# Optimization experiments

Measured on AMD Instinct MI355X. Metric: run time of the kernel, lower is better.

The kernel has to match this reference:

```python
import math
import jax, jax.numpy as jnp
import numpy as np

B, S, D = 4, 2048, 512
N_HEADS, D_HEAD = 8, 64
NUM_BUCKETS, MAX_DIST = 32, 128


def _relative_position_bucket(relative_position, num_buckets=NUM_BUCKETS, max_distance=MAX_DIST):
    # bidirectional variant (is_decoder=False)
    num_buckets = num_buckets // 2
    rel_buckets = (relative_position > 0).astype(jnp.int32) * num_buckets
    rp = jnp.abs(relative_position)
    max_exact = num_buckets // 2
    is_small = rp < max_exact
    rp_large = max_exact + (
        jnp.log(rp.astype(jnp.float32) / max_exact)
        / math.log(max_distance / max_exact)
        * (num_buckets - max_exact)
    ).astype(jnp.int32)
    rp_large = jnp.minimum(rp_large, num_buckets - 1)
    return rel_buckets + jnp.where(is_small, rp, rp_large)


def compute_bias(rel_bias, q_len, k_len):
    ctx = jnp.arange(q_len)[:, None]
    mem = jnp.arange(k_len)[None, :]
    buckets = _relative_position_bucket(mem - ctx)           # [q, k]
    values = rel_bias[buckets]                                # [q, k, h]
    return jnp.transpose(values, (2, 0, 1))[None]             # [1, h, q, k]


def setup_inputs() -> dict:
    key = jax.random.key(0)
    ks = jax.random.split(key, 6)
    scale = 1.0 / math.sqrt(D)
    return {
        "hidden_states": jax.random.normal(ks[0], (B, S, D), jnp.float32),
        "Wq": jax.random.normal(ks[1], (D, D), jnp.float32) * scale,
        "Wk": jax.random.normal(ks[2], (D, D), jnp.float32) * scale,
        "Wv": jax.random.normal(ks[3], (D, D), jnp.float32) * scale,
        "Wo": jax.random.normal(ks[4], (D, D), jnp.float32) * scale,
        "rel_bias": jax.random.normal(ks[5], (NUM_BUCKETS, N_HEADS), jnp.float32),
    }


def reference(hidden_states, Wq, Wk, Wv, Wo, rel_bias):
    b, s, _ = hidden_states.shape
    # projections (no bias, no 1/sqrt(d) scaling — T5 style)
    q = (hidden_states @ Wq).reshape(b, s, N_HEADS, D_HEAD).transpose(0, 2, 1, 3)
    k = (hidden_states @ Wk).reshape(b, s, N_HEADS, D_HEAD).transpose(0, 2, 1, 3)
    v = (hidden_states @ Wv).reshape(b, s, N_HEADS, D_HEAD).transpose(0, 2, 1, 3)
    scores = jnp.einsum("bhqd,bhkd->bhqk", q, k)             # [b,h,s,s]
    position_bias = compute_bias(rel_bias, s, s)              # [1,h,s,s]
    scores = scores + position_bias
    attn = jax.nn.softmax(scores, axis=-1)                    # dropout: eval mode -> identity
    out = jnp.einsum("bhqk,bhkd->bhqd", attn, v)
    out = out.transpose(0, 2, 1, 3).reshape(b, s, N_HEADS * D_HEAD)
    return out @ Wo
```

## Files before the change

kernel.cpp:

```cpp
#include <hip/hip_runtime.h>
#include <stdint.h>

typedef __attribute__((ext_vector_type(8))) __bf16 bf16x8;
typedef __attribute__((ext_vector_type(4))) __bf16 bf16x4;
typedef __attribute__((ext_vector_type(8))) _Float16 f16x8;
typedef __attribute__((ext_vector_type(4))) float f32x4;
typedef __attribute__((ext_vector_type(4))) unsigned int u32x4;

#define SEQ 2048
#define LOG2E 1.4426950408889634f

#define OFF_HSF   0ull
#define OFF_AO    0ull
#define OFF_WF    8388608ull
#define OFF_WO    9961472ull
#define OFF_Q     10485760ull
#define OFF_K     18874368ull
#define OFF_VT    27262976ull
#define OFF_BIAS  35651584ull

__device__ __forceinline__ int swz(int row) { return ((row & 7) << 4) ^ ((row & 8) << 1); }

__device__ __forceinline__ void gl_lds16(const void* g, void* l) {
  __builtin_amdgcn_global_load_lds(
      (__attribute__((address_space(1))) void*)(uintptr_t)g,
      (__attribute__((address_space(3))) void*)(uint32_t)(uintptr_t)l, 16, 0, 0);
}

__device__ __forceinline__ float fast_exp2(float x) { return __builtin_amdgcn_exp2f(x); }

__global__ void k_prep(const float* __restrict__ hs,
                       const float* __restrict__ Wq, const float* __restrict__ Wk,
                       const float* __restrict__ Wv, const float* __restrict__ Wo,
                       const float* __restrict__ rel_bias,
                       _Float16* __restrict__ hsf, _Float16* __restrict__ wf,
                       __bf16* __restrict__ wo_t, float* __restrict__ bias_tab) {
  int z = blockIdx.z;
  if (z >= 4) {
    int cid = (z - 4) * 64 + blockIdx.y * 8 + blockIdx.x;
    int gid = cid * 256 + threadIdx.x;
    int row = gid >> 6, c8 = (gid & 63) * 8;
    const float* p = hs + (size_t)row * 512 + c8;
    float4 a = *(const float4*)p, b = *(const float4*)(p + 4);
    float v[8] = {a.x, a.y, a.z, a.w, b.x, b.y, b.z, b.w};
    f16x8 hv;
#pragma unroll
    for (int j = 0; j < 8; ++j) hv[j] = (_Float16)v[j];
    *(f16x8*)(hsf + (size_t)row * 512 + c8) = hv;
    return;
  }
  __shared__ float tile[64][65];
  const float* W = (z == 0) ? Wq : (z == 1) ? Wk : (z == 2) ? Wv : Wo;
  int k0 = blockIdx.y * 64, n0 = blockIdx.x * 64;
  int tx = threadIdx.x & 63, ty = threadIdx.x >> 6;
  for (int r = ty; r < 64; r += 4) tile[r][tx] = W[(size_t)(k0 + r) * 512 + n0 + tx];
  __syncthreads();
  if (z < 3) {
    float scale = (z == 0) ? LOG2E : 1.0f;
    for (int r = ty; r < 64; r += 4)
      wf[(size_t)(z * 512 + n0 + r) * 512 + k0 + tx] = (_Float16)(tile[tx][r] * scale);
  } else {
    for (int r = ty; r < 64; r += 4)
      wo_t[(size_t)(n0 + r) * 512 + k0 + tx] = (__bf16)tile[tx][r];
    int blk = blockIdx.y * 8 + blockIdx.x;
#pragma unroll
    for (int e = 0; e < 2; ++e) {
      int idx = blk * 512 + e * 256 + threadIdx.x;
      int h = idx >> 12, dIdx = idx & 4095;
      float v = 0.f;
      if (dIdx < 4095) {
        int d = dIdx - 2047;
        int rp = d < 0 ? -d : d;
        int bp;
        if (rp < 8) bp = rp;
        else bp = 8 + (rp >= 12) + (rp >= 16) + (rp >= 23) + (rp >= 32) + (rp >= 46) + (rp >= 64) + (rp >= 91);
        v = rel_bias[((d > 0 ? 16 : 0) + bp) * 8 + h] * LOG2E;
      }
      bias_tab[idx] = v;
    }
  }
}

template <int MODE, int KSTEPS, int LDA, int LDB>
__global__ __launch_bounds__(256) void k_gemm(const void* __restrict__ Ap,
                                              const void* __restrict__ Btp,
                                              _Float16* __restrict__ qf,
                                              _Float16* __restrict__ kf,
                                              __bf16* __restrict__ vt,
                                              float* __restrict__ fo) {
  __shared__ __align__(16) char As[2][128 * 32 * 2];
  __shared__ __align__(16) char Bs[2][128 * 32 * 2];
  const char* A = (const char*)Ap;
  const char* Bt = (const char*)Btp;
  int tid = threadIdx.x, w = tid >> 6, l = tid & 63;
  int lr = l & 15, lh = l >> 4;
  int nwg = gridDim.x * gridDim.y;
  int flat = blockIdx.y * gridDim.x + blockIdx.x;
  int flat2 = (flat & 7) * (nwg >> 3) + (flat >> 3);
  int m0 = (flat2 / gridDim.x) * 128, n0 = (flat2 % gridDim.x) * 128;
  int wm = (w >> 1) * 64, wn = (w & 1) * 64;
  f32x4 zero4 = {0.f, 0.f, 0.f, 0.f};
  f32x4 acc[4][4];
#pragma unroll
  for (int i = 0; i < 4; ++i)
#pragma unroll
    for (int j = 0; j < 4; ++j) acc[i][j] = zero4;

  auto stage = [&](int kt, int buf) {
#pragma unroll
    for (int c = 0; c < 2; ++c) {
      int i = c * 256 + w * 64 + l;
      int row = i >> 2, cc = i & 3;
      gl_lds16(A + ((size_t)(m0 + row) * LDA + kt * 32 + cc * 8) * 2,
               &As[buf][(c * 256 + w * 64) * 16]);
      gl_lds16(Bt + ((size_t)(n0 + row) * LDB + kt * 32 + cc * 8) * 2,
               &Bs[buf][(c * 256 + w * 64) * 16]);
    }
  };

  stage(0, 0);
  __syncthreads();
#pragma unroll 2
  for (int kt = 0; kt < KSTEPS; ++kt) {
    int cur = kt & 1;
    if (kt + 1 < KSTEPS) stage(kt + 1, cur ^ 1);
    u32x4 af[4], bfr[4];
#pragma unroll
    for (int mi = 0; mi < 4; ++mi)
      af[mi] = *(const u32x4*)&As[cur][((wm + mi * 16 + lr) * 32 + lh * 8) * 2];
#pragma unroll
    for (int ni = 0; ni < 4; ++ni)
      bfr[ni] = *(const u32x4*)&Bs[cur][((wn + ni * 16 + lr) * 32 + lh * 8) * 2];
#pragma unroll
    for (int mi = 0; mi < 4; ++mi)
#pragma unroll
      for (int ni = 0; ni < 4; ++ni) {
        if (MODE == 0)
          acc[mi][ni] = __builtin_amdgcn_mfma_f32_16x16x32_f16(
              __builtin_bit_cast(f16x8, af[mi]), __builtin_bit_cast(f16x8, bfr[ni]),
              acc[mi][ni], 0, 0, 0);
        else
          acc[mi][ni] = __builtin_amdgcn_mfma_f32_16x16x32_bf16(
              __builtin_bit_cast(bf16x8, af[mi]), __builtin_bit_cast(bf16x8, bfr[ni]),
              acc[mi][ni], 0, 0, 0);
      }
    __syncthreads();
  }

  if (MODE == 0 && n0 >= 1024) {
#pragma unroll
    for (int mi = 0; mi < 4; ++mi)
#pragma unroll
      for (int ni = 0; ni < 4; ++ni) {
        int m = m0 + wm + mi * 16 + lh * 4;
        int n = n0 + wn + ni * 16 + lr;
        int c9 = n & 511, hh = c9 >> 6, dh = c9 & 63;
        int b = m >> 11, s = m & 2047;
        int loc = s & 63;
        int pp = ((loc >> 5) << 5) | (((loc >> 2) & 3) << 3) | (((loc >> 4) & 1) << 2);
        bf16x4 o;
#pragma unroll
        for (int r = 0; r < 4; ++r) o[r] = (__bf16)acc[mi][ni][r];
        *(bf16x4*)&vt[((size_t)(b * 8 + hh) * 64 + dh) * 2048 + (s & ~63) + pp] = o;
      }
    return;
  }

#pragma unroll
  for (int mi = 0; mi < 4; ++mi)
#pragma unroll
    for (int ni = 0; ni < 4; ++ni)
#pragma unroll
      for (int r = 0; r < 4; ++r) {
        int m = m0 + wm + mi * 16 + lh * 4 + r;
        int n = n0 + wn + ni * 16 + lr;
        float vv = acc[mi][ni][r];
        if (MODE == 0) {
          int which = n >> 9, c9 = n & 511, hh = c9 >> 6, dh = c9 & 63;
          int b = m >> 11, s = m & 2047;
          size_t o = (size_t)((b * 8 + hh) * 2048 + s) * 64 + dh;
          if (which == 0) qf[o] = (_Float16)vv;
          else            kf[o] = (_Float16)vv;
        } else {
          fo[(size_t)m * 512 + n] = vv;
        }
      }
}

__global__ __launch_bounds__(512) void k_attn(const _Float16* __restrict__ qfp,
                                              const _Float16* __restrict__ kfp,
                                              const __bf16* __restrict__ vt,
                                              const float* __restrict__ bias_tab,
                                              __bf16* __restrict__ ao) {
  __shared__ __align__(16) char Ks[4][64 * 128];
  __shared__ __align__(16) char Vs[4][64 * 128];
  __shared__ float bias_s[2304];
  int tid = threadIdx.x, w = tid >> 6, l = tid & 63;
  int lr = l & 15, lh = l >> 4;
  int d = blockIdx.x;
  int bh = (d & 7) + ((d >> 3) & 3) * 8;
  int q0 = (d >> 5) * 256;
  int h = bh & 7, b = bh >> 3;
  const char* kbase = (const char*)(kfp + (size_t)bh * SEQ * 64);
  const char* vbase = (const char*)(vt + (size_t)bh * 64 * SEQ);

  float bR = bias_tab[h * 4096 + 2047 + 200];
  float bL = bias_tab[h * 4096 + 2047 - 200];

  for (int j = tid; j < 2304; j += 512)
    bias_s[j] = bias_tab[h * 4096 + (1792 - q0) + j];

  auto stageKV = [&](int kt, int buf) {
    const char* kb = kbase + (size_t)kt * 64 * 128;
    const char* vb = vbase + (size_t)kt * 128;
    int row = tid >> 3, colb = (tid & 7) * 16;
    gl_lds16(kb + row * 128 + (colb ^ swz(row)), &Ks[buf][tid * 16]);
    gl_lds16(vb + (size_t)row * 4096 + (colb ^ swz(row)), &Vs[buf][tid * 16]);
  };

  f16x8 qf[2][2];
#pragma unroll
  for (int qs = 0; qs < 2; ++qs) {
    int qrow = w * 32 + qs * 16 + lr;
    const _Float16* qg = qfp + ((size_t)bh * SEQ + q0 + qrow) * 64;
    qf[qs][0] = *(const f16x8*)(qg + lh * 8);
    qf[qs][1] = *(const f16x8*)(qg + 32 + lh * 8);
  }

  float l_run0 = 0.f, l_run1 = 0.f;
  f32x4 zero4 = {0.f, 0.f, 0.f, 0.f};
  f32x4 oacc[2][4];
#pragma unroll
  for (int qs = 0; qs < 2; ++qs)
#pragma unroll
    for (int i = 0; i < 4; ++i) oacc[qs][i] = zero4;

  auto qk = [&](int kt, int buf, f32x4 (&sacc)[2][4]) {
    int dmin = kt * 64 - q0 - 255, dmax = kt * 64 + 63 - q0;
    bool far = (dmin >= 91) || (dmax <= -91);
    f32x4 cinit[2][4];
    if (far) {
      float cb = (dmin >= 91) ? bR : bL;
#pragma unroll
      for (int qs = 0; qs < 2; ++qs)
#pragma unroll
        for (int t = 0; t < 4; ++t)
#pragma unroll
          for (int r = 0; r < 4; ++r) cinit[qs][t][r] = cb;
    } else {
#pragma unroll
      for (int qs = 0; qs < 2; ++qs) {
        int jb = kt * 64 + lh * 4 + 255 - (w * 32 + qs * 16 + lr);
#pragma unroll
        for (int t = 0; t < 4; ++t)
#pragma unroll
          for (int r = 0; r < 4; ++r) cinit[qs][t][r] = bias_s[jb + t * 16 + r];
      }
    }
    const char* kb = &Ks[buf][0];
    __builtin_amdgcn_s_setprio(1);
#pragma unroll
    for (int t = 0; t < 4; ++t) {
      int row = t * 16 + lr;
      f16x8 b0 = *(const f16x8*)(kb + row * 128 + ((lh * 16) ^ swz(row)));
      f16x8 b1 = *(const f16x8*)(kb + row * 128 + ((64 + lh * 16) ^ swz(row)));
#pragma unroll
      for (int qs = 0; qs < 2; ++qs) {
        f32x4 z = cinit[qs][t];
        z = __builtin_amdgcn_mfma_f32_16x16x32_f16(b0, qf[qs][0], z, 0, 0, 0);
        z = __builtin_amdgcn_mfma_f32_16x16x32_f16(b1, qf[qs][1], z, 0, 0, 0);
        sacc[qs][t] = z;
      }
    }
    __builtin_amdgcn_s_setprio(0);
  };

  auto finish = [&](int buf, f32x4 (&sacc)[2][4]) {
    bf16x8 paA[2], paB[2];
#pragma unroll
    for (int qs = 0; qs < 2; ++qs) {
      float p[4][4];
      float rt[4];
#pragma unroll
      for (int t = 0; t < 4; ++t) {
#pragma unroll
        for (int r = 0; r < 4; ++r) p[t][r] = fast_exp2(sacc[qs][t][r]);
        rt[t] = (p[t][0] + p[t][1]) + (p[t][2] + p[t][3]);
      }
      if (qs == 0) l_run0 += (rt[0] + rt[1]) + (rt[2] + rt[3]);
      else         l_run1 += (rt[0] + rt[1]) + (rt[2] + rt[3]);
      uint32_t pk[4][2];
#pragma unroll
      for (int t = 0; t < 4; ++t) {
        asm("v_cvt_pk_bf16_f32 %0, %1, %2" : "=v"(pk[t][0]) : "v"(p[t][0]), "v"(p[t][1]));
        asm("v_cvt_pk_bf16_f32 %0, %1, %2" : "=v"(pk[t][1]) : "v"(p[t][2]), "v"(p[t][3]));
      }
      u32x4 A0 = {pk[0][0], pk[0][1], pk[1][0], pk[1][1]};
      u32x4 A1 = {pk[2][0], pk[2][1], pk[3][0], pk[3][1]};
      paA[qs] = __builtin_bit_cast(bf16x8, A0);
      paB[qs] = __builtin_bit_cast(bf16x8, A1);
    }
    const char* vbr = &Vs[buf][0];
    __builtin_amdgcn_s_setprio(1);
#pragma unroll
    for (int ni = 0; ni < 4; ++ni) {
      int vrow = ni * 16 + lr;
      bf16x8 v0 = *(const bf16x8*)(vbr + vrow * 128 + ((lh * 16) ^ swz(vrow)));
      bf16x8 v1 = *(const bf16x8*)(vbr + vrow * 128 + ((64 + lh * 16) ^ swz(vrow)));
#pragma unroll
      for (int qs = 0; qs < 2; ++qs) {
        oacc[qs][ni] = __builtin_amdgcn_mfma_f32_16x16x32_bf16(paA[qs], v0, oacc[qs][ni], 0, 0, 0);
        oacc[qs][ni] = __builtin_amdgcn_mfma_f32_16x16x32_bf16(paB[qs], v1, oacc[qs][ni], 0, 0, 0);
      }
    }
    __builtin_amdgcn_s_setprio(0);
  };

  stageKV(0, 0);
  stageKV(1, 1);
  __syncthreads();
  f32x4 sA[2][4], sB[2][4];
#pragma unroll 2
  for (int kp = 0; kp < 16; ++kp) {
    int rb_ = (kp & 1) * 2;
    qk(2 * kp, rb_, sA);
    qk(2 * kp + 1, rb_ + 1, sB);
    if (kp < 15) {
      stageKV(2 * kp + 2, rb_ ^ 2);
      stageKV(2 * kp + 3, (rb_ ^ 2) + 1);
    }
    finish(rb_, sA);
    finish(rb_ + 1, sB);
    __syncthreads();
  }

  l_run0 += __shfl_xor(l_run0, 16);
  l_run0 += __shfl_xor(l_run0, 32);
  l_run1 += __shfl_xor(l_run1, 16);
  l_run1 += __shfl_xor(l_run1, 32);

#pragma unroll
  for (int qs = 0; qs < 2; ++qs) {
    float lsel = (qs == 0) ? l_run0 : l_run1;
#pragma unroll
    for (int r = 0; r < 4; ++r) {
      float linv = 1.0f / __shfl(lsel, lh * 4 + r);
      int s = q0 + w * 32 + qs * 16 + lh * 4 + r;
#pragma unroll
      for (int ni = 0; ni < 4; ++ni) {
        int dh = ni * 16 + lr;
        ao[((size_t)(b * 2048 + s)) * 512 + h * 64 + dh] = (__bf16)(oacc[qs][ni][r] * linv);
      }
    }
  }
}

extern "C" void kernel_launch(void* const* d_in, const int* in_sizes, int n_in,
                              void* d_out, int out_size, void* d_ws, size_t ws_size,
                              hipStream_t stream) {
  (void)in_sizes; (void)n_in; (void)out_size; (void)ws_size;
  const float* hs = (const float*)d_in[0];
  const float* Wq = (const float*)d_in[1];
  const float* Wk = (const float*)d_in[2];
  const float* Wv = (const float*)d_in[3];
  const float* Wo = (const float*)d_in[4];
  const float* rb = (const float*)d_in[5];
  char* ws = (char*)d_ws;
  _Float16* hsf  = (_Float16*)(ws + OFF_HSF);
  _Float16* wfb  = (_Float16*)(ws + OFF_WF);
  __bf16* wo_t   = (__bf16*)(ws + OFF_WO);
  _Float16* qfb  = (_Float16*)(ws + OFF_Q);
  _Float16* kfb  = (_Float16*)(ws + OFF_K);
  __bf16* vtb    = (__bf16*)(ws + OFF_VT);
  __bf16* aob    = (__bf16*)(ws + OFF_AO);
  float*  bias   = (float*)(ws + OFF_BIAS);

  k_prep<<<dim3(8, 8, 36), 256, 0, stream>>>(hs, Wq, Wk, Wv, Wo, rb, hsf, wfb, wo_t, bias);
  k_gemm<0, 16, 512, 512><<<dim3(12, 64), 256, 0, stream>>>(hsf, wfb, qfb, kfb, vtb, nullptr);
  k_attn<<<dim3(256), 512, 0, stream>>>(qfb, kfb, vtb, bias, aob);
  k_gemm<1, 16, 512, 512><<<dim3(4, 64), 256, 0, stream>>>(aob, wo_t, nullptr, nullptr, nullptr, (float*)d_out);
}
```

Baseline: 89.99 us.

## Fuse fp32->fp16 input conversion into QKV GEMM and deepen attention KV pipeline

The separate conversion of hidden_states to fp16 in the prep kernel is removed. The QKV GEMM now loads the fp32 activations directly, converts them in registers and writes them to LDS, which saves a full write and re-read of the fp16 copy. Separately, the attention kernel moves from 4 to 6 KV LDS buffers and skews the loop so that the softmax finish of the previous odd tile overlaps the next QK products. The costs are more LDS use, which can lower occupancy, and synchronous loads in the GEMM A path where async LDS loads were used before.

Measured after the change: 88.17 us. 2.0% less time.

```diff
diff --git a/kernel.cpp b/kernel.cpp
--- a/kernel.cpp
+++ b/kernel.cpp
@@ -10,7 +10,6 @@
 #define SEQ 2048
 #define LOG2E 1.4426950408889634f
 
-#define OFF_HSF   0ull
 #define OFF_AO    0ull
 #define OFF_WF    8388608ull
 #define OFF_WO    9961472ull
@@ -29,26 +28,12 @@
 
 __device__ __forceinline__ float fast_exp2(float x) { return __builtin_amdgcn_exp2f(x); }
 
-__global__ void k_prep(const float* __restrict__ hs,
-                       const float* __restrict__ Wq, const float* __restrict__ Wk,
+__global__ void k_prep(const float* __restrict__ Wq, const float* __restrict__ Wk,
                        const float* __restrict__ Wv, const float* __restrict__ Wo,
                        const float* __restrict__ rel_bias,
-                       _Float16* __restrict__ hsf, _Float16* __restrict__ wf,
-                       __bf16* __restrict__ wo_t, float* __restrict__ bias_tab) {
+                       _Float16* __restrict__ wf, __bf16* __restrict__ wo_t,
+                       float* __restrict__ bias_tab) {
   int z = blockIdx.z;
-  if (z >= 4) {
-    int cid = (z - 4) * 64 + blockIdx.y * 8 + blockIdx.x;
-    int gid = cid * 256 + threadIdx.x;
-    int row = gid >> 6, c8 = (gid & 63) * 8;
-    const float* p = hs + (size_t)row * 512 + c8;
-    float4 a = *(const float4*)p, b = *(const float4*)(p + 4);
-    float v[8] = {a.x, a.y, a.z, a.w, b.x, b.y, b.z, b.w};
-    f16x8 hv;
-#pragma unroll
-    for (int j = 0; j < 8; ++j) hv[j] = (_Float16)v[j];
-    *(f16x8*)(hsf + (size_t)row * 512 + c8) = hv;
-    return;
-  }
   __shared__ float tile[64][65];
   const float* W = (z == 0) ? Wq : (z == 1) ? Wk : (z == 2) ? Wv : Wo;
   int k0 = blockIdx.y * 64, n0 = blockIdx.x * 64;
@@ -90,8 +75,6 @@
                                               float* __restrict__ fo) {
   __shared__ __align__(16) char As[2][128 * 32 * 2];
   __shared__ __align__(16) char Bs[2][128 * 32 * 2];
-  const char* A = (const char*)Ap;
-  const char* Bt = (const char*)Btp;
   int tid = threadIdx.x, w = tid >> 6, l = tid & 63;
   int lr = l & 15, lh = l >> 4;
   int nwg = gridDim.x * gridDim.y;
@@ -107,14 +90,38 @@
     for (int j = 0; j < 4; ++j) acc[i][j] = zero4;
 
   auto stage = [&](int kt, int buf) {
-#pragma unroll
-    for (int c = 0; c < 2; ++c) {
-      int i = c * 256 + w * 64 + l;
-      int row = i >> 2, cc = i & 3;
-      gl_lds16(A + ((size_t)(m0 + row) * LDA + kt * 32 + cc * 8) * 2,
-               &As[buf][(c * 256 + w * 64) * 16]);
-      gl_lds16(Bt + ((size_t)(n0 + row) * LDB + kt * 32 + cc * 8) * 2,
-               &Bs[buf][(c * 256 + w * 64) * 16]);
+    if (MODE == 0) {
+      const float* Af = (const float*)Ap;
+#pragma unroll
+      for (int c = 0; c < 2; ++c) {
+        int i = c * 256 + tid;
+        int row = i >> 2, cc = i & 3;
+        const float* src = Af + (size_t)(m0 + row) * LDA + kt * 32 + cc * 8;
+        float4 a = *(const float4*)src, b2 = *(const float4*)(src + 4);
+        f16x8 hv;
+        hv[0] = (_Float16)a.x;  hv[1] = (_Float16)a.y;
+        hv[2] = (_Float16)a.z;  hv[3] = (_Float16)a.w;
+        hv[4] = (_Float16)b2.x; hv[5] = (_Float16)b2.y;
+        hv[6] = (_Float16)b2.z; hv[7] = (_Float16)b2.w;
+        *(f16x8*)&As[buf][i * 16] = hv;
+      }
+#pragma unroll
+      for (int c = 0; c < 2; ++c) {
+        int i = c * 256 + tid;
+        int row = i >> 2, cc = i & 3;
+        gl_lds16((const char*)Btp + ((size_t)(n0 + row) * LDB + kt * 32 + cc * 8) * 2,
+                 &Bs[buf][i * 16]);
+      }
+    } else {
+#pragma unroll
+      for (int c = 0; c < 2; ++c) {
+        int i = c * 256 + tid;
+        int row = i >> 2, cc = i & 3;
+        gl_lds16((const char*)Ap + ((size_t)(m0 + row) * LDA + kt * 32 + cc * 8) * 2,
+                 &As[buf][i * 16]);
+        gl_lds16((const char*)Btp + ((size_t)(n0 + row) * LDB + kt * 32 + cc * 8) * 2,
+                 &Bs[buf][i * 16]);
+      }
     }
   };
 
@@ -192,8 +199,8 @@
                                               const __bf16* __restrict__ vt,
                                               const float* __restrict__ bias_tab,
                                               __bf16* __restrict__ ao) {
-  __shared__ __align__(16) char Ks[4][64 * 128];
-  __shared__ __align__(16) char Vs[4][64 * 128];
+  __shared__ __align__(16) char Ks[6][64 * 128];
+  __shared__ __align__(16) char Vs[6][64 * 128];
   __shared__ float bias_s[2304];
   int tid = threadIdx.x, w = tid >> 6, l = tid & 63;
   int lr = l & 15, lh = l >> 4;
@@ -319,20 +326,25 @@
   stageKV(0, 0);
   stageKV(1, 1);
   __syncthreads();
-  f32x4 sA[2][4], sB[2][4];
+  f32x4 sA[2][4], sB0[2][4], sB1[2][4];
 #pragma unroll 2
   for (int kp = 0; kp < 16; ++kp) {
-    int rb_ = (kp & 1) * 2;
-    qk(2 * kp, rb_, sA);
-    qk(2 * kp + 1, rb_ + 1, sB);
-    if (kp < 15) {
-      stageKV(2 * kp + 2, rb_ ^ 2);
-      stageKV(2 * kp + 3, (rb_ ^ 2) + 1);
-    }
-    finish(rb_, sA);
-    finish(rb_ + 1, sB);
+    if (kp <= 14) {
+      stageKV(2 * kp + 2, (2 * kp + 2) % 6);
+      stageKV(2 * kp + 3, (2 * kp + 3) % 6);
+    }
+    qk(2 * kp, (2 * kp) % 6, sA);
+    if (kp & 1) {
+      qk(2 * kp + 1, (2 * kp + 1) % 6, sB1);
+      if (kp >= 1) finish((2 * kp - 1) % 6, sB0);
+    } else {
+      qk(2 * kp + 1, (2 * kp + 1) % 6, sB0);
+      if (kp >= 1) finish((2 * kp - 1) % 6, sB1);
+    }
+    finish((2 * kp) % 6, sA);
     __syncthreads();
   }
+  finish(31 % 6, sB1);
 
   l_run0 += __shfl_xor(l_run0, 16);
   l_run0 += __shfl_xor(l_run0, 32);
@@ -366,7 +378,6 @@
   const float* Wo = (const float*)d_in[4];
   const float* rb = (const float*)d_in[5];
   char* ws = (char*)d_ws;
-  _Float16* hsf  = (_Float16*)(ws + OFF_HSF);
   _Float16* wfb  = (_Float16*)(ws + OFF_WF);
   __bf16* wo_t   = (__bf16*)(ws + OFF_WO);
   _Float16* qfb  = (_Float16*)(ws + OFF_Q);
@@ -375,8 +386,8 @@
   __bf16* aob    = (__bf16*)(ws + OFF_AO);
   float*  bias   = (float*)(ws + OFF_BIAS);
 
-  k_prep<<<dim3(8, 8, 36), 256, 0, stream>>>(hs, Wq, Wk, Wv, Wo, rb, hsf, wfb, wo_t, bias);
-  k_gemm<0, 16, 512, 512><<<dim3(12, 64), 256, 0, stream>>>(hsf, wfb, qfb, kfb, vtb, nullptr);
+  k_prep<<<dim3(8, 8, 4), 256, 0, stream>>>(Wq, Wk, Wv, Wo, rb, wfb, wo_t, bias);
+  k_gemm<0, 16, 512, 512><<<dim3(12, 64), 256, 0, stream>>>(hs, wfb, qfb, kfb, vtb, nullptr);
   k_attn<<<dim3(256), 512, 0, stream>>>(qfb, kfb, vtb, bias, aob);
   k_gemm<1, 16, 512, 512><<<dim3(4, 64), 256, 0, stream>>>(aob, wo_t, nullptr, nullptr, nullptr, (float*)d_out);
 }
```
